# Kernel optimization log

Measured on AMD Instinct MI355X. Metric: run time of the kernel, lower is better.

The kernel has to match this reference:

```python
import jax, jax.numpy as jnp
import numpy as np

THR = 0.2          # config['thr']
BORDER_RM = 2      # config['border_rm']
TEMP = 0.1         # config['dsmax_temperature']


def setup_inputs() -> dict:
    key = jax.random.key(0)
    k0, k1 = jax.random.split(key)
    N, C = 2, 256
    h0c, w0c, h1c, w1c = 60, 80, 60, 80
    return {
        "feat_c0": jax.random.normal(k0, (N, h0c * w0c, C), dtype=jnp.float32),
        "feat_c1": jax.random.normal(k1, (N, h1c * w1c, C), dtype=jnp.float32),
        "h0c": h0c, "w0c": w0c, "h1c": h1c, "w1c": w1c,
    }


def _valid_1d(n: int, b: int):
    # True in the interior [b, n-b), False on the border — matches mask_border writes
    return jnp.zeros((n,), dtype=bool).at[b:n - b].set(True)


def reference(feat_c0, feat_c1, h0c, w0c, h1c, w1c):
    N, L, C = feat_c0.shape
    S = feat_c1.shape[1]
    scale = 1.0 / (C ** 0.5)
    f0 = feat_c0 * scale
    f1 = feat_c1 * scale

    # similarity + dual softmax  -> conf_matrix [N, L, S]
    sim = jnp.einsum('nlc,nsc->nls', f0, f1) / TEMP
    conf = jax.nn.softmax(sim, axis=1) * jax.nn.softmax(sim, axis=2)

    # threshold + border removal (mask_border, vectorized as an interior mask)
    mask = conf > THR
    b = BORDER_RM
    border = (_valid_1d(h0c, b)[:, None, None, None]
              & _valid_1d(w0c, b)[None, :, None, None]
              & _valid_1d(h1c, b)[None, None, :, None]
              & _valid_1d(w1c, b)[None, None, None, :])  # [h0c,w0c,h1c,w1c]
    mask = (mask.reshape(N, h0c, w0c, h1c, w1c) & border[None]).reshape(N, L, S)

    # mutual nearest neighbor
    mask = mask \
        & (conf == conf.max(axis=2, keepdims=True)) \
        & (conf == conf.max(axis=1, keepdims=True))

    # match extraction, expressed densely (static shapes for jit):
    # mask_v[b,i] = row i of pair b has a match; j_ids its column; mconf its confidence
    mask_v = mask.any(axis=2)                               # [N, L]
    j_ids = jnp.argmax(mask, axis=2)                        # [N, L] (first True)
    mconf = jnp.take_along_axis(conf, j_ids[:, :, None], axis=2)[..., 0]
    mconf = jnp.where(mask_v, mconf, 0.0)                   # [N, L]

    # coarse keypoint coords for matched columns: (x, y) = (j % w1c, j // w1c)
    mkpts1_c = jnp.stack([j_ids % w1c, j_ids // w1c], axis=-1)  # [N, L, 2]

    return conf, mask_v, j_ids, mkpts1_c, mconf
```

## Files before the change

### kernel.cpp

```cpp
#include <hip/hip_runtime.h>

typedef _Float16 half8 __attribute__((ext_vector_type(8)));
typedef float f32x4 __attribute__((ext_vector_type(4)));

#define NB 2
#define LS 4800
#define CCH 256
#define W0 80
#define W1 80
#define THRV 0.2f
#define SQS 0.19764235376052370f

#define TN 38
#define PADL 4864

#define OF_RST  0
#define OF_CST  19200
#define OF_RWM  38400
#define OF_CAND 48000
#define OF_CLM  57600
#define OF_PROW 67200
#define OF_PCOL (67200 + 739328)
#define OF_AH   (67200 + 2*739328)
#define OF_BH   (OF_AH + 1228800)

#define O_MASKV 46080000ull
#define O_JIDS  46089600ull
#define O_MKPT  46099200ull
#define O_MCONF 46118400ull

__device__ __forceinline__ void load_lds16(const void* g, void* l) {
    __builtin_amdgcn_global_load_lds((const __attribute__((address_space(1))) void*)g,
                                     (__attribute__((address_space(3))) void*)l, 16, 0, 0);
}

__global__ __launch_bounds__(256) void conv_half(const float* __restrict__ A,
                                                 const float* __restrict__ B,
                                                 float* __restrict__ ws) {
    const int which = blockIdx.y;
    const float* src = which ? B : A;
    _Float16* dst = (_Float16*)(ws + (which ? OF_BH : OF_AH));
    const int idx = blockIdx.x * 256 + threadIdx.x;
    const float4 v = ((const float4*)src)[idx];
    union { _Float16 h[4]; uint2 u; } p;
    p.h[0] = (_Float16)(v.x * SQS);
    p.h[1] = (_Float16)(v.y * SQS);
    p.h[2] = (_Float16)(v.z * SQS);
    p.h[3] = (_Float16)(v.w * SQS);
    ((uint2*)dst)[idx] = p.u;
}

__device__ __forceinline__ void gemm_core(const _Float16* __restrict__ Ah,
                                          const _Float16* __restrict__ Bh,
                                          _Float16* smA, _Float16* smB,
                                          const int bx, const int by,
                                          const int tid, f32x4 (&acc)[4][4]) {
    const int lane = tid & 63, w = tid >> 6;
    const int wx = w & 1, wy = w >> 1;
    const int m = lane & 15, quad = lane >> 4;
    const int srow = lane >> 3;
    const int qst = (lane & 7) ^ (srow & 7);

    for (int kt = 0; kt < 4; kt++) {
        const int k0 = kt * 64;
#pragma unroll
        for (int i = 0; i < 4; i++) {
            const int c = i * 4 + w;
            int gr = by * 128 + c * 8 + srow; gr = gr < LS ? gr : LS - 1;
            load_lds16(Ah + (size_t)gr * CCH + k0 + qst * 8, &smA[c * 512]);
        }
#pragma unroll
        for (int i = 0; i < 4; i++) {
            const int c = i * 4 + w;
            int gr = bx * 128 + c * 8 + srow; gr = gr < LS ? gr : LS - 1;
            load_lds16(Bh + (size_t)gr * CCH + k0 + qst * 8, &smB[c * 512]);
        }
        __syncthreads();
#pragma unroll
        for (int t = 0; t < 2; t++) {
            half8 Af[4], Bf[4];
#pragma unroll
            for (int a = 0; a < 4; a++) {
                const int rl = wy * 64 + a * 16 + m;
                const int sl = rl * 8 + ((t * 4 + quad) ^ (rl & 7));
                Af[a] = *(const half8*)&smA[sl * 8];
            }
#pragma unroll
            for (int b = 0; b < 4; b++) {
                const int cl = wx * 64 + b * 16 + m;
                const int sl = cl * 8 + ((t * 4 + quad) ^ (cl & 7));
                Bf[b] = *(const half8*)&smB[sl * 8];
            }
#pragma unroll
            for (int a = 0; a < 4; a++)
#pragma unroll
                for (int b = 0; b < 4; b++)
                    acc[a][b] = __builtin_amdgcn_mfma_f32_16x16x32_f16(Af[a], Bf[b], acc[a][b], 0, 0, 0);
        }
        __syncthreads();
    }
}

__global__ __launch_bounds__(256, 2) void gemm_stats(float* __restrict__ ws) {
    __shared__ __align__(16) union {
        struct { _Float16 A[8192]; _Float16 B[8192]; } st;
        struct { float rs[128][2][2]; float cs[128][2][2]; } red;
    } sm;
    const int bx = blockIdx.x, by = blockIdx.y, n = blockIdx.z;
    const _Float16* Ah = (const _Float16*)(ws + OF_AH) + (size_t)n * LS * CCH;
    const _Float16* Bh = (const _Float16*)(ws + OF_BH) + (size_t)n * LS * CCH;
    const int tid = threadIdx.x;
    const int lane = tid & 63, w = tid >> 6;
    const int wx = w & 1, wy = w >> 1;
    const int m = lane & 15, quad = lane >> 4;

    f32x4 acc[4][4];
    {
        f32x4 z = {0.f, 0.f, 0.f, 0.f};
#pragma unroll
        for (int a = 0; a < 4; a++)
#pragma unroll
            for (int b = 0; b < 4; b++) acc[a][b] = z;
    }
    gemm_core(Ah, Bh, sm.st.A, sm.st.B, bx, by, tid, acc);

    const int l0 = by * 128, s0 = bx * 128;
    bool bval[4];
#pragma unroll
    for (int b = 0; b < 4; b++) bval[b] = (s0 + wx * 64 + b * 16 + m) < LS;

    float T = -1e30f;
#pragma unroll
    for (int a = 0; a < 4; a++)
#pragma unroll
        for (int reg = 0; reg < 4; reg++) {
            if ((l0 + wy * 64 + a * 16 + quad * 4 + reg) < LS) {
#pragma unroll
                for (int b = 0; b < 4; b++)
                    if (bval[b]) T = fmaxf(T, acc[a][b][reg]);
            }
        }
#pragma unroll
    for (int d = 1; d < 64; d <<= 1) T = fmaxf(T, __shfl_xor(T, d, 64));

#pragma unroll
    for (int a = 0; a < 4; a++)
#pragma unroll
        for (int reg = 0; reg < 4; reg++) {
            const bool rv = (l0 + wy * 64 + a * 16 + quad * 4 + reg) < LS;
#pragma unroll
            for (int b = 0; b < 4; b++)
                acc[a][b][reg] = (rv && bval[b]) ? __expf(acc[a][b][reg] - T) : 0.f;
        }

#pragma unroll
    for (int a = 0; a < 4; a++)
#pragma unroll
        for (int reg = 0; reg < 4; reg++) {
            float s = acc[a][0][reg] + acc[a][1][reg] + acc[a][2][reg] + acc[a][3][reg];
#pragma unroll
            for (int d = 1; d < 16; d <<= 1) s += __shfl_xor(s, d, 64);
            if (m == 0) {
                const int rl = wy * 64 + a * 16 + quad * 4 + reg;
                sm.red.rs[rl][wx][0] = T; sm.red.rs[rl][wx][1] = s;
            }
        }
#pragma unroll
    for (int b = 0; b < 4; b++) {
        float s = 0.f;
#pragma unroll
        for (int a = 0; a < 4; a++)
#pragma unroll
            for (int reg = 0; reg < 4; reg++) s += acc[a][b][reg];
        s += __shfl_xor(s, 16, 64);
        s += __shfl_xor(s, 32, 64);
        if (quad == 0) {
            const int cl = wx * 64 + b * 16 + m;
            sm.red.cs[cl][wy][0] = T; sm.red.cs[cl][wy][1] = s;
        }
    }
    __syncthreads();
    if (tid < 128) {
        const float m0 = sm.red.rs[tid][0][0], v0 = sm.red.rs[tid][0][1];
        const float m1 = sm.red.rs[tid][1][0], v1 = sm.red.rs[tid][1][1];
        const float nm = fmaxf(m0, m1);
        const float s = v0 * __expf(m0 - nm) + v1 * __expf(m1 - nm);
        ((float2*)(ws + OF_PROW))[((size_t)n * TN + bx) * PADL + by * 128 + tid] = make_float2(nm, s);
    } else {
        const int t = tid - 128;
        const float m0 = sm.red.cs[t][0][0], v0 = sm.red.cs[t][0][1];
        const float m1 = sm.red.cs[t][1][0], v1 = sm.red.cs[t][1][1];
        const float nm = fmaxf(m0, m1);
        const float s = v0 * __expf(m0 - nm) + v1 * __expf(m1 - nm);
        ((float2*)(ws + OF_PCOL))[((size_t)n * TN + by) * PADL + bx * 128 + t] = make_float2(nm, s);
    }
}

__global__ __launch_bounds__(256) void combine_stats(float* __restrict__ ws) {
    const int idx = blockIdx.x * 256 + threadIdx.x;
    const int half_ = idx >= 9600;
    const int i = idx - half_ * 9600;
    const int n = i / LS, r = i % LS;
    const float2* P = (const float2*)(ws + (half_ ? OF_PCOL : OF_PROW)) + (size_t)n * TN * PADL + r;
    float M = -1e30f, S = 0.f;
    for (int b = 0; b < TN; b++) {
        const float2 p = P[(size_t)b * PADL];
        const float nm = fmaxf(M, p.x);
        S = S * __expf(M - nm) + p.y * __expf(p.x - nm);
        M = nm;
    }
    ((float2*)(ws + (half_ ? OF_CST : OF_RST)))[n * LS + r] = make_float2(M, 1.0f / S);
}

__global__ __launch_bounds__(256, 2) void gemm_conf(float* __restrict__ out,
                                                    float* __restrict__ ws) {
    __shared__ __align__(16) union {
        struct { _Float16 A[8192]; _Float16 B[8192]; } st;
        struct { float rst[128][2]; float cst[128][2];
                 float rsv[128][2][2]; float csv[128][2]; } ep;
    } sm;
    const int bx = blockIdx.x, by = blockIdx.y, n = blockIdx.z;
    const _Float16* Ah = (const _Float16*)(ws + OF_AH) + (size_t)n * LS * CCH;
    const _Float16* Bh = (const _Float16*)(ws + OF_BH) + (size_t)n * LS * CCH;
    const int tid = threadIdx.x;
    const int lane = tid & 63, w = tid >> 6;
    const int wx = w & 1, wy = w >> 1;
    const int m = lane & 15, quad = lane >> 4;

    f32x4 acc[4][4];
    {
        f32x4 z = {0.f, 0.f, 0.f, 0.f};
#pragma unroll
        for (int a = 0; a < 4; a++)
#pragma unroll
            for (int b = 0; b < 4; b++) acc[a][b] = z;
    }
    gemm_core(Ah, Bh, sm.st.A, sm.st.B, bx, by, tid, acc);

    const int l0 = by * 128, s0 = bx * 128;
    if (tid < 128) {
        int r = l0 + tid; r = r < LS ? r : LS - 1;
        const float2 v = ((const float2*)(ws + OF_RST))[n * LS + r];
        sm.ep.rst[tid][0] = v.x; sm.ep.rst[tid][1] = v.y;
    } else {
        const int t = tid - 128;
        int c = s0 + t; c = c < LS ? c : LS - 1;
        const float2 v = ((const float2*)(ws + OF_CST))[n * LS + c];
        sm.ep.cst[t][0] = v.x; sm.ep.cst[t][1] = v.y;
    }
    __syncthreads();

    float* On = out + (size_t)n * LS * LS;
    float colm[4] = {-1.f, -1.f, -1.f, -1.f};
    bool bval[4]; int gc4[4]; float cmx[4], csi[4];
#pragma unroll
    for (int b = 0; b < 4; b++) {
        const int cl = wx * 64 + b * 16 + m;
        gc4[b] = s0 + cl;
        bval[b] = gc4[b] < LS;
        cmx[b] = sm.ep.cst[cl][0]; csi[b] = sm.ep.cst[cl][1];
    }
#pragma unroll
    for (int a = 0; a < 4; a++) {
#pragma unroll
        for (int reg = 0; reg < 4; reg++) {
            const int rl = wy * 64 + a * 16 + quad * 4 + reg;
            const int gr = l0 + rl;
            const float rm = sm.ep.rst[rl][0], rsi = sm.ep.rst[rl][1];
            const bool rv = gr < LS;
            float bestv = -1.f; int besti = 0;
#pragma unroll
            for (int b = 0; b < 4; b++) {
                const float c = __expf(2.f * acc[a][b][reg] - rm - cmx[b]) * (rsi * csi[b]);
                if (rv && bval[b]) {
                    On[(size_t)gr * LS + gc4[b]] = c;
                    if (c > bestv) { bestv = c; besti = gc4[b]; }
                    colm[b] = fmaxf(colm[b], c);
                }
            }
#pragma unroll
            for (int d = 1; d < 16; d <<= 1) {
                const float ov = __shfl_xor(bestv, d, 64);
                const int oi = __shfl_xor(besti, d, 64);
                if (ov > bestv || (ov == bestv && oi < besti)) { bestv = ov; besti = oi; }
            }
            if (m == 0) {
                sm.ep.rsv[rl][wx][0] = bestv;
                sm.ep.rsv[rl][wx][1] = __int_as_float(besti);
            }
        }
    }
#pragma unroll
    for (int b = 0; b < 4; b++) {
        float v = colm[b];
        v = fmaxf(v, __shfl_xor(v, 16, 64));
        v = fmaxf(v, __shfl_xor(v, 32, 64));
        if (quad == 0) sm.ep.csv[wx * 64 + b * 16 + m][wy] = v;
    }
    __syncthreads();
    if (tid < 128) {
        const float v0 = sm.ep.rsv[tid][0][0]; const int i0 = __float_as_int(sm.ep.rsv[tid][0][1]);
        const float v1 = sm.ep.rsv[tid][1][0]; const int i1 = __float_as_int(sm.ep.rsv[tid][1][1]);
        float bv; int bi;
        if (v0 > v1 || (v0 == v1 && i0 <= i1)) { bv = v0; bi = i0; } else { bv = v1; bi = i1; }
        ((float2*)(ws + OF_PROW))[((size_t)n * TN + bx) * PADL + by * 128 + tid] =
            make_float2(bv, __int_as_float(bi));
    } else {
        const int t = tid - 128;
        const float v = fmaxf(sm.ep.csv[t][0], sm.ep.csv[t][1]);
        (ws + OF_PCOL)[((size_t)n * TN + by) * PADL + bx * 128 + t] = v;
    }
}

__global__ __launch_bounds__(256) void combine_max(float* __restrict__ ws) {
    const int idx = blockIdx.x * 256 + threadIdx.x;
    const int half_ = idx >= 9600;
    const int i = idx - half_ * 9600;
    const int n = i / LS, r = i % LS;
    if (!half_) {
        const float2* P = (const float2*)(ws + OF_PROW) + (size_t)n * TN * PADL + r;
        float bv = -2.f; int bi = 0;
        for (int b = 0; b < TN; b++) {
            const float2 p = P[(size_t)b * PADL];
            const int pi = __float_as_int(p.y);
            if (p.x > bv || (p.x == bv && pi < bi)) { bv = p.x; bi = pi; }
        }
        ws[OF_RWM + i] = bv;
        ((int*)ws)[OF_CAND + i] = bi;
    } else {
        const float* P = ws + OF_PCOL + (size_t)n * TN * PADL + r;
        float v = -2.f;
        for (int b = 0; b < TN; b++) v = fmaxf(v, P[(size_t)b * PADL]);
        ws[OF_CLM + i] = v;
    }
}

__global__ __launch_bounds__(256) void match_pass(const float* __restrict__ ws,
                                                  float* __restrict__ out) {
    const int idx = blockIdx.x * 256 + threadIdx.x;
    if (idx >= NB * LS) return;
    const int n = idx / LS, l = idx % LS;
    const float rwm = ws[OF_RWM + idx];
    const int cand = ((const int*)ws)[OF_CAND + idx];
    const float clm = ws[OF_CLM + n * LS + cand];
    const int y0 = l / W0, x0 = l % W0;
    const int y1 = cand / W1, x1 = cand % W1;
    const bool b0 = (y0 >= 2 && y0 < 58 && x0 >= 2 && x0 < 78);
    const bool b1 = (y1 >= 2 && y1 < 58 && x1 >= 2 && x1 < 78);
    const bool matched = (rwm > THRV) && b0 && b1 && (rwm == clm);
    const int j = matched ? cand : 0;
    out[O_MASKV + idx] = matched ? 1.f : 0.f;
    out[O_JIDS + idx] = (float)j;
    out[O_MKPT + (size_t)idx * 2 + 0] = (float)(j % W1);
    out[O_MKPT + (size_t)idx * 2 + 1] = (float)(j / W1);
    out[O_MCONF + idx] = matched ? rwm : 0.f;
}

extern "C" void kernel_launch(void* const* d_in, const int* in_sizes, int n_in,
                              void* d_out, int out_size, void* d_ws, size_t ws_size,
                              hipStream_t stream) {
    const float* f0 = (const float*)d_in[0];
    const float* f1 = (const float*)d_in[1];
    float* out = (float*)d_out;
    float* ws = (float*)d_ws;

    conv_half<<<dim3(2400, 2), 256, 0, stream>>>(f0, f1, ws);
    gemm_stats<<<dim3(TN, TN, NB), 256, 0, stream>>>(ws);
    combine_stats<<<75, 256, 0, stream>>>(ws);
    gemm_conf<<<dim3(TN, TN, NB), 256, 0, stream>>>(out, ws);
    combine_max<<<75, 256, 0, stream>>>(ws);
    match_pass<<<38, 256, 0, stream>>>(ws, out);
}
```

Baseline: 306.8 us.

## Double-buffer LDS tiles in GEMM core and transpose partial-stat layout

The GEMM main loop now uses two LDS buffers: it prefetches the next K-slice into the alternate buffer while MFMAs consume the current one, which drops one barrier per iteration. This targets the load-compute serialization in both GEMM passes. It doubles the shared memory per block, which could reduce occupancy. Separately, the per-tile partial row/column statistics are stored tile-index-minor, so each combine thread reads its partials contiguously, but the GEMM epilogue writes become strided.

```diff
diff --git a/kernel.cpp b/kernel.cpp
--- a/kernel.cpp
+++ b/kernel.cpp
@@ -61,21 +61,37 @@
     const int srow = lane >> 3;
     const int qst = (lane & 7) ^ (srow & 7);
 
+    const _Float16* ga[4];
+    const _Float16* gb[4];
+#pragma unroll
+    for (int i = 0; i < 4; i++) {
+        const int c = i * 4 + w;
+        int gra = by * 128 + c * 8 + srow; gra = gra < LS ? gra : LS - 1;
+        int grb = bx * 128 + c * 8 + srow; grb = grb < LS ? grb : LS - 1;
+        ga[i] = Ah + (size_t)gra * CCH + qst * 8;
+        gb[i] = Bh + (size_t)grb * CCH + qst * 8;
+    }
+
+#pragma unroll
+    for (int i = 0; i < 4; i++) {
+        const int c = i * 4 + w;
+        load_lds16(ga[i], &smA[c * 512]);
+        load_lds16(gb[i], &smB[c * 512]);
+    }
+
     for (int kt = 0; kt < 4; kt++) {
-        const int k0 = kt * 64;
-#pragma unroll
-        for (int i = 0; i < 4; i++) {
-            const int c = i * 4 + w;
-            int gr = by * 128 + c * 8 + srow; gr = gr < LS ? gr : LS - 1;
-            load_lds16(Ah + (size_t)gr * CCH + k0 + qst * 8, &smA[c * 512]);
-        }
-#pragma unroll
-        for (int i = 0; i < 4; i++) {
-            const int c = i * 4 + w;
-            int gr = bx * 128 + c * 8 + srow; gr = gr < LS ? gr : LS - 1;
-            load_lds16(Bh + (size_t)gr * CCH + k0 + qst * 8, &smB[c * 512]);
-        }
         __syncthreads();
+        const int cur = (kt & 1) * 8192;
+        if (kt < 3) {
+            const int nxt = 8192 - cur;
+            const int ko = (kt + 1) * 64;
+#pragma unroll
+            for (int i = 0; i < 4; i++) {
+                const int c = i * 4 + w;
+                load_lds16(ga[i] + ko, &smA[nxt + c * 512]);
+                load_lds16(gb[i] + ko, &smB[nxt + c * 512]);
+            }
+        }
 #pragma unroll
         for (int t = 0; t < 2; t++) {
             half8 Af[4], Bf[4];
@@ -83,13 +99,13 @@
             for (int a = 0; a < 4; a++) {
                 const int rl = wy * 64 + a * 16 + m;
                 const int sl = rl * 8 + ((t * 4 + quad) ^ (rl & 7));
-                Af[a] = *(const half8*)&smA[sl * 8];
+                Af[a] = *(const half8*)&smA[cur + sl * 8];
             }
 #pragma unroll
             for (int b = 0; b < 4; b++) {
                 const int cl = wx * 64 + b * 16 + m;
                 const int sl = cl * 8 + ((t * 4 + quad) ^ (cl & 7));
-                Bf[b] = *(const half8*)&smB[sl * 8];
+                Bf[b] = *(const half8*)&smB[cur + sl * 8];
             }
 #pragma unroll
             for (int a = 0; a < 4; a++)
@@ -97,13 +113,13 @@
                 for (int b = 0; b < 4; b++)
                     acc[a][b] = __builtin_amdgcn_mfma_f32_16x16x32_f16(Af[a], Bf[b], acc[a][b], 0, 0, 0);
         }
-        __syncthreads();
-    }
+    }
+    __syncthreads();
 }
 
 __global__ __launch_bounds__(256, 2) void gemm_stats(float* __restrict__ ws) {
     __shared__ __align__(16) union {
-        struct { _Float16 A[8192]; _Float16 B[8192]; } st;
+        struct { _Float16 A[2][8192]; _Float16 B[2][8192]; } st;
         struct { float rs[128][2][2]; float cs[128][2][2]; } red;
     } sm;
     const int bx = blockIdx.x, by = blockIdx.y, n = blockIdx.z;
@@ -122,7 +138,7 @@
 #pragma unroll
             for (int b = 0; b < 4; b++) acc[a][b] = z;
     }
-    gemm_core(Ah, Bh, sm.st.A, sm.st.B, bx, by, tid, acc);
+    gemm_core(Ah, Bh, &sm.st.A[0][0], &sm.st.B[0][0], bx, by, tid, acc);
 
     const int l0 = by * 128, s0 = bx * 128;
     bool bval[4];
@@ -185,14 +201,14 @@
         const float m1 = sm.red.rs[tid][1][0], v1 = sm.red.rs[tid][1][1];
         const float nm = fmaxf(m0, m1);
         const float s = v0 * __expf(m0 - nm) + v1 * __expf(m1 - nm);
-        ((float2*)(ws + OF_PROW))[((size_t)n * TN + bx) * PADL + by * 128 + tid] = make_float2(nm, s);
+        ((float2*)(ws + OF_PROW))[((size_t)n * PADL + by * 128 + tid) * TN + bx] = make_float2(nm, s);
     } else {
         const int t = tid - 128;
         const float m0 = sm.red.cs[t][0][0], v0 = sm.red.cs[t][0][1];
         const float m1 = sm.red.cs[t][1][0], v1 = sm.red.cs[t][1][1];
         const float nm = fmaxf(m0, m1);
         const float s = v0 * __expf(m0 - nm) + v1 * __expf(m1 - nm);
-        ((float2*)(ws + OF_PCOL))[((size_t)n * TN + by) * PADL + bx * 128 + t] = make_float2(nm, s);
+        ((float2*)(ws + OF_PCOL))[((size_t)n * PADL + bx * 128 + t) * TN + by] = make_float2(nm, s);
     }
 }
 
@@ -201,10 +217,10 @@
     const int half_ = idx >= 9600;
     const int i = idx - half_ * 9600;
     const int n = i / LS, r = i % LS;
-    const float2* P = (const float2*)(ws + (half_ ? OF_PCOL : OF_PROW)) + (size_t)n * TN * PADL + r;
+    const float2* P = (const float2*)(ws + (half_ ? OF_PCOL : OF_PROW)) + ((size_t)n * PADL + r) * TN;
     float M = -1e30f, S = 0.f;
     for (int b = 0; b < TN; b++) {
-        const float2 p = P[(size_t)b * PADL];
+        const float2 p = P[b];
         const float nm = fmaxf(M, p.x);
         S = S * __expf(M - nm) + p.y * __expf(p.x - nm);
         M = nm;
@@ -215,7 +231,7 @@
 __global__ __launch_bounds__(256, 2) void gemm_conf(float* __restrict__ out,
                                                     float* __restrict__ ws) {
     __shared__ __align__(16) union {
-        struct { _Float16 A[8192]; _Float16 B[8192]; } st;
+        struct { _Float16 A[2][8192]; _Float16 B[2][8192]; } st;
         struct { float rst[128][2]; float cst[128][2];
                  float rsv[128][2][2]; float csv[128][2]; } ep;
     } sm;
@@ -235,7 +251,7 @@
 #pragma unroll
             for (int b = 0; b < 4; b++) acc[a][b] = z;
     }
-    gemm_core(Ah, Bh, sm.st.A, sm.st.B, bx, by, tid, acc);
+    gemm_core(Ah, Bh, &sm.st.A[0][0], &sm.st.B[0][0], bx, by, tid, acc);
 
     const int l0 = by * 128, s0 = bx * 128;
     if (tid < 128) {
@@ -303,12 +319,12 @@
         const float v1 = sm.ep.rsv[tid][1][0]; const int i1 = __float_as_int(sm.ep.rsv[tid][1][1]);
         float bv; int bi;
         if (v0 > v1 || (v0 == v1 && i0 <= i1)) { bv = v0; bi = i0; } else { bv = v1; bi = i1; }
-        ((float2*)(ws + OF_PROW))[((size_t)n * TN + bx) * PADL + by * 128 + tid] =
+        ((float2*)(ws + OF_PROW))[((size_t)n * PADL + by * 128 + tid) * TN + bx] =
             make_float2(bv, __int_as_float(bi));
     } else {
         const int t = tid - 128;
         const float v = fmaxf(sm.ep.csv[t][0], sm.ep.csv[t][1]);
-        (ws + OF_PCOL)[((size_t)n * TN + by) * PADL + bx * 128 + t] = v;
+        (ws + OF_PCOL)[((size_t)n * PADL + bx * 128 + t) * TN + by] = v;
     }
 }
 
@@ -318,19 +334,19 @@
     const int i = idx - half_ * 9600;
     const int n = i / LS, r = i % LS;
     if (!half_) {
-        const float2* P = (const float2*)(ws + OF_PROW) + (size_t)n * TN * PADL + r;
+        const float2* P = (const float2*)(ws + OF_PROW) + ((size_t)n * PADL + r) * TN;
         float bv = -2.f; int bi = 0;
         for (int b = 0; b < TN; b++) {
-            const float2 p = P[(size_t)b * PADL];
+            const float2 p = P[b];
             const int pi = __float_as_int(p.y);
             if (p.x > bv || (p.x == bv && pi < bi)) { bv = p.x; bi = pi; }
         }
         ws[OF_RWM + i] = bv;
         ((int*)ws)[OF_CAND + i] = bi;
     } else {
-        const float* P = ws + OF_PCOL + (size_t)n * TN * PADL + r;
+        const float* P = ws + OF_PCOL + ((size_t)n * PADL + r) * TN;
         float v = -2.f;
-        for (int b = 0; b < TN; b++) v = fmaxf(v, P[(size_t)b * PADL]);
+        for (int b = 0; b < TN; b++) v = fmaxf(v, P[b]);
         ws[OF_CLM + i] = v;
     }
 }
```

Result: slower. 343.4 us (+11.9%).
